# Kernel optimization log

Hardware: AMD Instinct MI355X
Metric: run time of the kernel (lower is better)

The kernel has to match this reference:

```python
import jax, jax.numpy as jnp
import numpy as np

EPS = 1e-12


def _complex_log(x):
    # log of a real tensor as a complex number: log|x| + i*pi*[x<0]
    real = jnp.log(jnp.maximum(jnp.abs(x), EPS))
    imag = jnp.where(x < 0, jnp.pi, 0.0).astype(jnp.float32)
    return jax.lax.complex(real.astype(jnp.float32), imag)


def _logcumsumexp_complex(x, axis):
    # numerically-stable complex logcumsumexp via associative scan
    def logaddexp_c(a, b):
        m = jnp.maximum(a.real, b.real)  # real-valued max for stability
        return jnp.log(jnp.exp(a - m) + jnp.exp(b - m)) + m
    return jax.lax.associative_scan(logaddexp_c, x, axis=axis)


def setup_inputs() -> dict:
    key = jax.random.key(0)
    ks = jax.random.split(key, 7)
    b, d, l, n = 2, 1024, 1024, 16
    u = jax.random.normal(ks[0], (b, d, l), dtype=jnp.float32)
    delta = jax.random.normal(ks[1], (b, d, l), dtype=jnp.float32)
    # A negative (like Mamba's A = -exp(A_log)) so the scan stays stable
    A = -(0.5 + jax.random.uniform(ks[2], (d, n), dtype=jnp.float32))
    B = jax.random.normal(ks[3], (b, n, l), dtype=jnp.float32)
    C = jax.random.normal(ks[4], (b, n, l), dtype=jnp.float32)
    D = jax.random.normal(ks[5], (d,), dtype=jnp.float32)
    z = jax.random.normal(ks[6], (b, d, l), dtype=jnp.float32)
    return {"u": u, "delta": delta, "A": A, "B": B, "C": C, "D": D, "z": z}


def reference(u, delta, A, B, C, D, z):
    # delta_softplus=True path of SelectiveScanTorch.forward
    dt = jax.nn.softplus(delta)                                   # (b,d,l)
    dA = jnp.einsum('bdl,dn->bldn', dt, A)                        # (b,l,d,n)
    dB_u = jnp.einsum('bdl,bdl,bnl->bldn', dt, u, B)              # (b,l,d,n)

    dB_u_log = _complex_log(dB_u)                                 # complex64
    # dA_star[l] = sum_{k=1}^{l} dA[k]  (exclusive of step 0, front-padded)
    dA_star = jnp.pad(jnp.cumsum(dA[:, 1:], axis=1),
                      ((0, 0), (1, 0), (0, 0), (0, 0)))
    x_log = _logcumsumexp_complex(dB_u_log - dA_star, axis=1) + dA_star

    x_real = jnp.exp(x_log.real) * jnp.cos(x_log.imag)            # (b,l,d,n)
    y = jnp.einsum('bldn,bnl->bdl', x_real.astype(C.dtype), C)    # (b,d,l)
    out = y + u * D[None, :, None]
    return (out * jax.nn.silu(z)).astype(u.dtype)
```

## Files before the change

### kernel.cpp

```cpp
#include <hip/hip_runtime.h>
#include <math.h>

namespace {

constexpr int kD = 1024;
constexpr int kL = 1024;
constexpr int kN = 16;
constexpr int kE = 8;
constexpr int kJ = 8;
constexpr int kT = 256;

__global__ __launch_bounds__(kT)
void selscan(const float* __restrict__ u,
             const float* __restrict__ delta,
             const float* __restrict__ A,
             const float* __restrict__ Bm,
             const float* __restrict__ Cm,
             const float* __restrict__ Dv,
             const float* __restrict__ z,
             float* __restrict__ out)
{
    __shared__ float2 sax[128][kN + 1];

    const int bd   = blockIdx.x;
    const int b    = bd >> 10;
    const int d    = bd & (kD - 1);
    const int t    = threadIdx.x;
    const int lane = t & 63;
    const int wave = t >> 6;
    const int nh   = t & 1;
    const int n0   = nh << 3;
    const int chunk = t >> 1;
    const int l0   = chunk << 3;
    const size_t base = (size_t)bd * kL;

    const float LOG2E = 1.4426950408889634f;
    const float LN2   = 0.6931471805599453f;

    float dt[kE], dtu[kE];
    {
        float4 d0 = *(const float4*)(delta + base + l0);
        float4 d1 = *(const float4*)(delta + base + l0 + 4);
        float4 u0 = *(const float4*)(u + base + l0);
        float4 u1 = *(const float4*)(u + base + l0 + 4);
        float dd[kE] = {d0.x,d0.y,d0.z,d0.w,d1.x,d1.y,d1.z,d1.w};
        float uu[kE] = {u0.x,u0.y,u0.z,u0.w,u1.x,u1.y,u1.z,u1.w};
        #pragma unroll
        for (int s = 0; s < kE; ++s) {
            float x = dd[s];
            float e = __builtin_amdgcn_exp2f(-fabsf(x) * LOG2E);
            float sp = fmaxf(x, 0.f) + __builtin_amdgcn_logf(1.f + e) * LN2;
            dt[s]  = sp;
            dtu[s] = sp * uu[s];
        }
    }

    float cj[kJ];
    {
        float4 a0 = *(const float4*)(A + d * kN + n0);
        float4 a1 = *(const float4*)(A + d * kN + n0 + 4);
        cj[0]=a0.x*LOG2E; cj[1]=a0.y*LOG2E; cj[2]=a0.z*LOG2E; cj[3]=a0.w*LOG2E;
        cj[4]=a1.x*LOG2E; cj[5]=a1.y*LOG2E; cj[6]=a1.z*LOG2E; cj[7]=a1.w*LOG2E;
    }

    float Q[kJ][kE];
    float y[kE] = {0.f,0.f,0.f,0.f,0.f,0.f,0.f,0.f};
    const int rowbase = (b << 4) + n0;
    #pragma unroll
    for (int j = 0; j < kJ; ++j) {
        const float* Bp = Bm + (size_t)(rowbase + j) * kL + l0;
        const float* Cp = Cm + (size_t)(rowbase + j) * kL + l0;
        float4 b0 = *(const float4*)Bp;
        float4 b1 = *(const float4*)(Bp + 4);
        float4 c0 = *(const float4*)Cp;
        float4 c1 = *(const float4*)(Cp + 4);
        float Bv[kE] = {b0.x,b0.y,b0.z,b0.w,b1.x,b1.y,b1.z,b1.w};
        float Cv[kE] = {c0.x,c0.y,c0.z,c0.w,c1.x,c1.y,c1.z,c1.w};
        float x = 0.f, p = 1.f;
        #pragma unroll
        for (int s = 0; s < kE; ++s) {
            float e = __builtin_amdgcn_exp2f(dt[s] * cj[j]);
            x = fmaf(e, x, dtu[s] * Bv[s]);
            p *= e;
            Q[j][s] = p * Cv[s];
            y[s] = fmaf(x, Cv[s], y[s]);
        }
        sax[chunk][n0 + j] = make_float2(p, x);
    }
    __syncthreads();

    if (wave == 0) {
        const int sn = lane & 15;
        const int q  = lane >> 4;
        const int cb = q << 5;
        float p = 1.f, c = 0.f;
        #pragma unroll 8
        for (int i = 0; i < 32; ++i) {
            float2 ax = sax[cb + i][sn];
            c = fmaf(ax.x, c, ax.y);
            p *= ax.x;
        }
        float Ag = p, Xg = c;
        {
            float ain = __shfl_up(Ag, 16, 64);
            float xin = __shfl_up(Xg, 16, 64);
            bool act = (lane >= 16);
            Xg = fmaf(Ag, act ? xin : 0.f, Xg);
            Ag *= act ? ain : 1.f;
            ain = __shfl_up(Ag, 32, 64);
            xin = __shfl_up(Xg, 32, 64);
            act = (lane >= 32);
            Xg = fmaf(Ag, act ? xin : 0.f, Xg);
            Ag *= act ? ain : 1.f;
        }
        float gx = __shfl_up(Xg, 16, 64);
        float cc = (lane >= 16) ? gx : 0.f;
        #pragma unroll 8
        for (int i = 0; i < 32; ++i) {
            float2 ax = sax[cb + i][sn];
            sax[cb + i][sn].x = cc;
            cc = fmaf(ax.x, cc, ax.y);
        }
    }
    __syncthreads();

    #pragma unroll
    for (int j = 0; j < kJ; ++j) {
        float carry = sax[chunk][n0 + j].x;
        #pragma unroll
        for (int s = 0; s < kE; ++s)
            y[s] = fmaf(carry, Q[j][s], y[s]);
    }

    #pragma unroll
    for (int s = 0; s < kE; ++s) y[s] += __shfl_xor(y[s], 1, 64);

    const float D_d = Dv[d];
    float y0, y1, y2, y3;
    if (nh == 0) { y0 = y[0]; y1 = y[1]; y2 = y[2]; y3 = y[3]; }
    else         { y0 = y[4]; y1 = y[5]; y2 = y[6]; y3 = y[7]; }

    const int eoff = l0 + nh * 4;
    float4 zv = *(const float4*)(z + base + eoff);
    float4 uv = *(const float4*)(u + base + eoff);
    float s0 = __builtin_amdgcn_rcpf(1.f + __builtin_amdgcn_exp2f(-zv.x * LOG2E));
    float s1 = __builtin_amdgcn_rcpf(1.f + __builtin_amdgcn_exp2f(-zv.y * LOG2E));
    float s2 = __builtin_amdgcn_rcpf(1.f + __builtin_amdgcn_exp2f(-zv.z * LOG2E));
    float s3 = __builtin_amdgcn_rcpf(1.f + __builtin_amdgcn_exp2f(-zv.w * LOG2E));
    float4 o;
    o.x = (y0 + uv.x * D_d) * zv.x * s0;
    o.y = (y1 + uv.y * D_d) * zv.y * s1;
    o.z = (y2 + uv.z * D_d) * zv.z * s2;
    o.w = (y3 + uv.w * D_d) * zv.w * s3;
    *(float4*)(out + base + eoff) = o;
}

}

extern "C" void kernel_launch(void* const* d_in, const int* in_sizes, int n_in,
                              void* d_out, int out_size, void* d_ws, size_t ws_size,
                              hipStream_t stream) {
    const float* u     = (const float*)d_in[0];
    const float* delta = (const float*)d_in[1];
    const float* A     = (const float*)d_in[2];
    const float* Bm    = (const float*)d_in[3];
    const float* Cm    = (const float*)d_in[4];
    const float* Dv    = (const float*)d_in[5];
    const float* z     = (const float*)d_in[6];
    float* out = (float*)d_out;

    dim3 grid(2 * kD);
    dim3 block(kT);
    hipLaunchKernelGGL(selscan, grid, block, 0, stream,
                       u, delta, A, Bm, Cm, Dv, z, out);
}
```

Before: 26.04 us.

## Split state dimension across four threads per chunk with 512-thread blocks

Each length chunk is now handled by four threads covering 4 state channels each, instead of two threads covering 8, and the block grows to 512 threads. This halves per-thread B/C loads and the size of the Q register array, lowering register pressure and raising the number of threads available to hide latency. The cost is computing softplus and delta*u redundantly four times instead of twice, plus an extra shuffle-reduce step. The epilogue now writes two outputs per thread and reuses u from registers instead of reloading it from global memory.

Result: slower. 47.81 us (+83.6%).

```diff
diff --git a/kernel.cpp b/kernel.cpp
--- a/kernel.cpp
+++ b/kernel.cpp
@@ -7,8 +7,8 @@
 constexpr int kL = 1024;
 constexpr int kN = 16;
 constexpr int kE = 8;
-constexpr int kJ = 8;
-constexpr int kT = 256;
+constexpr int kJ = 4;
+constexpr int kT = 512;
 
 __global__ __launch_bounds__(kT)
 void selscan(const float* __restrict__ u,
@@ -28,9 +28,9 @@
     const int t    = threadIdx.x;
     const int lane = t & 63;
     const int wave = t >> 6;
-    const int nh   = t & 1;
-    const int n0   = nh << 3;
-    const int chunk = t >> 1;
+    const int ng   = t & 3;
+    const int n0   = ng << 2;
+    const int chunk = t >> 2;
     const int l0   = chunk << 3;
     const size_t base = (size_t)bd * kL;
 
@@ -38,11 +38,12 @@
     const float LN2   = 0.6931471805599453f;
 
     float dt[kE], dtu[kE];
+    float4 u0, u1;
     {
         float4 d0 = *(const float4*)(delta + base + l0);
         float4 d1 = *(const float4*)(delta + base + l0 + 4);
-        float4 u0 = *(const float4*)(u + base + l0);
-        float4 u1 = *(const float4*)(u + base + l0 + 4);
+        u0 = *(const float4*)(u + base + l0);
+        u1 = *(const float4*)(u + base + l0 + 4);
         float dd[kE] = {d0.x,d0.y,d0.z,d0.w,d1.x,d1.y,d1.z,d1.w};
         float uu[kE] = {u0.x,u0.y,u0.z,u0.w,u1.x,u1.y,u1.z,u1.w};
         #pragma unroll
@@ -57,10 +58,8 @@
 
     float cj[kJ];
     {
-        float4 a0 = *(const float4*)(A + d * kN + n0);
-        float4 a1 = *(const float4*)(A + d * kN + n0 + 4);
-        cj[0]=a0.x*LOG2E; cj[1]=a0.y*LOG2E; cj[2]=a0.z*LOG2E; cj[3]=a0.w*LOG2E;
-        cj[4]=a1.x*LOG2E; cj[5]=a1.y*LOG2E; cj[6]=a1.z*LOG2E; cj[7]=a1.w*LOG2E;
+        float4 a4 = *(const float4*)(A + d * kN + n0);
+        cj[0]=a4.x*LOG2E; cj[1]=a4.y*LOG2E; cj[2]=a4.z*LOG2E; cj[3]=a4.w*LOG2E;
     }
 
     float Q[kJ][kE];
@@ -133,26 +132,26 @@
     }
 
     #pragma unroll
-    for (int s = 0; s < kE; ++s) y[s] += __shfl_xor(y[s], 1, 64);
+    for (int s = 0; s < kE; ++s) {
+        y[s] += __shfl_xor(y[s], 1, 64);
+        y[s] += __shfl_xor(y[s], 2, 64);
+    }
 
     const float D_d = Dv[d];
-    float y0, y1, y2, y3;
-    if (nh == 0) { y0 = y[0]; y1 = y[1]; y2 = y[2]; y3 = y[3]; }
-    else         { y0 = y[4]; y1 = y[5]; y2 = y[6]; y3 = y[7]; }
+    bool g2 = (ng & 2) != 0, g1 = (ng & 1) != 0;
+    float ya  = g2 ? (g1 ? y[6] : y[4]) : (g1 ? y[2] : y[0]);
+    float yb  = g2 ? (g1 ? y[7] : y[5]) : (g1 ? y[3] : y[1]);
+    float ue0 = g2 ? (g1 ? u1.z : u1.x) : (g1 ? u0.z : u0.x);
+    float ue1 = g2 ? (g1 ? u1.w : u1.y) : (g1 ? u0.w : u0.y);
 
-    const int eoff = l0 + nh * 4;
-    float4 zv = *(const float4*)(z + base + eoff);
-    float4 uv = *(const float4*)(u + base + eoff);
+    const int eo = 2 * t;
+    float2 zv = *(const float2*)(z + base + eo);
     float s0 = __builtin_amdgcn_rcpf(1.f + __builtin_amdgcn_exp2f(-zv.x * LOG2E));
     float s1 = __builtin_amdgcn_rcpf(1.f + __builtin_amdgcn_exp2f(-zv.y * LOG2E));
-    float s2 = __builtin_amdgcn_rcpf(1.f + __builtin_amdgcn_exp2f(-zv.z * LOG2E));
-    float s3 = __builtin_amdgcn_rcpf(1.f + __builtin_amdgcn_exp2f(-zv.w * LOG2E));
-    float4 o;
-    o.x = (y0 + uv.x * D_d) * zv.x * s0;
-    o.y = (y1 + uv.y * D_d) * zv.y * s1;
-    o.z = (y2 + uv.z * D_d) * zv.z * s2;
-    o.w = (y3 + uv.w * D_d) * zv.w * s3;
-    *(float4*)(out + base + eoff) = o;
+    float2 o;
+    o.x = (ya + ue0 * D_d) * zv.x * s0;
+    o.y = (yb + ue1 * D_d) * zv.y * s1;
+    *(float2*)(out + base + eo) = o;
 }
 
 }
```

## Recompute decay products from prefix dt sums instead of holding Q in registers

Applied to the files above, without the earlier changes.

Drops the 64-entry Q[j][s] register array that held cumulative decay times C across the block barrier. Instead it computes prefix sums of dt and, after the carry scan, recomputes each decay factor as exp2(T[s]*A) and reloads C from global memory. The u*D term is also computed early from the already-loaded u, so the second load of u is gone. The aim is lower register pressure and higher occupancy, at the cost of extra exp2 calls, a second read of C, and a small numerical difference from using exp of a sum instead of a product of exps.

New measurement: 31.12 us. 1.2x slower.

```diff
diff --git a/kernel.cpp b/kernel.cpp
--- a/kernel.cpp
+++ b/kernel.cpp
@@ -33,11 +33,15 @@
     const int chunk = t >> 1;
     const int l0   = chunk << 3;
     const size_t base = (size_t)bd * kL;
+    const int eoff = l0 + nh * 4;
 
     const float LOG2E = 1.4426950408889634f;
     const float LN2   = 0.6931471805599453f;
 
+    const float D_d = Dv[d];
+
     float dt[kE], dtu[kE];
+    float ue0, ue1, ue2, ue3;
     {
         float4 d0 = *(const float4*)(delta + base + l0);
         float4 d1 = *(const float4*)(delta + base + l0 + 4);
@@ -53,7 +57,16 @@
             dt[s]  = sp;
             dtu[s] = sp * uu[s];
         }
+        ue0 = (nh ? u1.x : u0.x) * D_d;
+        ue1 = (nh ? u1.y : u0.y) * D_d;
+        ue2 = (nh ? u1.z : u0.z) * D_d;
+        ue3 = (nh ? u1.w : u0.w) * D_d;
     }
+
+    float T[kE];
+    T[0] = dt[0];
+    #pragma unroll
+    for (int s = 1; s < kE; ++s) T[s] = T[s - 1] + dt[s];
 
     float cj[kJ];
     {
@@ -63,7 +76,6 @@
         cj[4]=a1.x*LOG2E; cj[5]=a1.y*LOG2E; cj[6]=a1.z*LOG2E; cj[7]=a1.w*LOG2E;
     }
 
-    float Q[kJ][kE];
     float y[kE] = {0.f,0.f,0.f,0.f,0.f,0.f,0.f,0.f};
     const int rowbase = (b << 4) + n0;
     #pragma unroll
@@ -76,16 +88,15 @@
         float4 c1 = *(const float4*)(Cp + 4);
         float Bv[kE] = {b0.x,b0.y,b0.z,b0.w,b1.x,b1.y,b1.z,b1.w};
         float Cv[kE] = {c0.x,c0.y,c0.z,c0.w,c1.x,c1.y,c1.z,c1.w};
-        float x = 0.f, p = 1.f;
+        float x = 0.f;
         #pragma unroll
         for (int s = 0; s < kE; ++s) {
             float e = __builtin_amdgcn_exp2f(dt[s] * cj[j]);
             x = fmaf(e, x, dtu[s] * Bv[s]);
-            p *= e;
-            Q[j][s] = p * Cv[s];
             y[s] = fmaf(x, Cv[s], y[s]);
         }
-        sax[chunk][n0 + j] = make_float2(p, x);
+        float a = __builtin_amdgcn_exp2f(T[kE - 1] * cj[j]);
+        sax[chunk][n0 + j] = make_float2(a, x);
     }
     __syncthreads();
 
@@ -126,32 +137,36 @@
 
     #pragma unroll
     for (int j = 0; j < kJ; ++j) {
+        const float* Cp = Cm + (size_t)(rowbase + j) * kL + l0;
+        float4 c0 = *(const float4*)Cp;
+        float4 c1 = *(const float4*)(Cp + 4);
+        float Cv[kE] = {c0.x,c0.y,c0.z,c0.w,c1.x,c1.y,c1.z,c1.w};
         float carry = sax[chunk][n0 + j].x;
         #pragma unroll
-        for (int s = 0; s < kE; ++s)
-            y[s] = fmaf(carry, Q[j][s], y[s]);
+        for (int s = 0; s < kE; ++s) {
+            float p = __builtin_amdgcn_exp2f(T[s] * cj[j]);
+            y[s] = fmaf(carry * p, Cv[s], y[s]);
+        }
     }
 
     #pragma unroll
     for (int s = 0; s < kE; ++s) y[s] += __shfl_xor(y[s], 1, 64);
 
-    const float D_d = Dv[d];
-    float y0, y1, y2, y3;
-    if (nh == 0) { y0 = y[0]; y1 = y[1]; y2 = y[2]; y3 = y[3]; }
-    else         { y0 = y[4]; y1 = y[5]; y2 = y[6]; y3 = y[7]; }
+    float y0 = nh ? y[4] : y[0];
+    float y1 = nh ? y[5] : y[1];
+    float y2 = nh ? y[6] : y[2];
+    float y3 = nh ? y[7] : y[3];
 
-    const int eoff = l0 + nh * 4;
     float4 zv = *(const float4*)(z + base + eoff);
-    float4 uv = *(const float4*)(u + base + eoff);
     float s0 = __builtin_amdgcn_rcpf(1.f + __builtin_amdgcn_exp2f(-zv.x * LOG2E));
     float s1 = __builtin_amdgcn_rcpf(1.f + __builtin_amdgcn_exp2f(-zv.y * LOG2E));
     float s2 = __builtin_amdgcn_rcpf(1.f + __builtin_amdgcn_exp2f(-zv.z * LOG2E));
     float s3 = __builtin_amdgcn_rcpf(1.f + __builtin_amdgcn_exp2f(-zv.w * LOG2E));
     float4 o;
-    o.x = (y0 + uv.x * D_d) * zv.x * s0;
-    o.y = (y1 + uv.y * D_d) * zv.y * s1;
-    o.z = (y2 + uv.z * D_d) * zv.z * s2;
-    o.w = (y3 + uv.w * D_d) * zv.w * s3;
+    o.x = (y0 + ue0) * zv.x * s0;
+    o.y = (y1 + ue1) * zv.y * s1;
+    o.z = (y2 + ue2) * zv.z * s2;
+    o.w = (y3 + ue3) * zv.w * s3;
     *(float4*)(out + base + eoff) = o;
 }
 
```

## Parallelize chunk-carry scan across all four waves with cross-wave combine

Applied to the files above, without the earlier changes.

The inter-chunk carry scan previously ran on wave 0 alone, with each lane walking 32 chunks serially in two passes. Now all four waves each take 32 chunks, split 8 per lane group, then combine their partial results through a small shared array and an extra barrier. This shortens the serial carry-propagation phase while the other waves would otherwise sit idle, at the cost of one more __syncthreads and a little extra shared memory traffic.

Result: slower. 27.51 us (+5.7%).

```diff
diff --git a/kernel.cpp b/kernel.cpp
--- a/kernel.cpp
+++ b/kernel.cpp
@@ -21,6 +21,7 @@
              float* __restrict__ out)
 {
     __shared__ float2 sax[128][kN + 1];
+    __shared__ float2 sw[4][kN];
 
     const int bd   = blockIdx.x;
     const int b    = bd >> 10;
@@ -89,34 +90,45 @@
     }
     __syncthreads();
 
-    if (wave == 0) {
+    {
         const int sn = lane & 15;
         const int q  = lane >> 4;
-        const int cb = q << 5;
+        const int cb = (wave << 5) + (q << 3);
+
         float p = 1.f, c = 0.f;
-        #pragma unroll 8
-        for (int i = 0; i < 32; ++i) {
+        #pragma unroll
+        for (int i = 0; i < 8; ++i) {
             float2 ax = sax[cb + i][sn];
             c = fmaf(ax.x, c, ax.y);
             p *= ax.x;
         }
-        float Ag = p, Xg = c;
+        float Aq = p, Xq = c;
         {
-            float ain = __shfl_up(Ag, 16, 64);
-            float xin = __shfl_up(Xg, 16, 64);
+            float ain = __shfl_up(Aq, 16, 64);
+            float xin = __shfl_up(Xq, 16, 64);
             bool act = (lane >= 16);
-            Xg = fmaf(Ag, act ? xin : 0.f, Xg);
-            Ag *= act ? ain : 1.f;
-            ain = __shfl_up(Ag, 32, 64);
-            xin = __shfl_up(Xg, 32, 64);
+            Xq = fmaf(Aq, act ? xin : 0.f, Xq);
+            Aq *= act ? ain : 1.f;
+            ain = __shfl_up(Aq, 32, 64);
+            xin = __shfl_up(Xq, 32, 64);
             act = (lane >= 32);
-            Xg = fmaf(Ag, act ? xin : 0.f, Xg);
-            Ag *= act ? ain : 1.f;
+            Xq = fmaf(Aq, act ? xin : 0.f, Xq);
+            Aq *= act ? ain : 1.f;
         }
-        float gx = __shfl_up(Xg, 16, 64);
-        float cc = (lane >= 16) ? gx : 0.f;
-        #pragma unroll 8
-        for (int i = 0; i < 32; ++i) {
+        if (q == 3) sw[wave][sn] = make_float2(Aq, Xq);
+        float eA = __shfl_up(Aq, 16, 64);
+        float eX = __shfl_up(Xq, 16, 64);
+        if (lane < 16) { eA = 1.f; eX = 0.f; }
+        __syncthreads();
+        float wx = 0.f;
+        if (wave > 0) {
+            wx = sw[0][sn].y;
+            if (wave > 1) { float2 s1 = sw[1][sn]; wx = fmaf(s1.x, wx, s1.y); }
+            if (wave > 2) { float2 s2 = sw[2][sn]; wx = fmaf(s2.x, wx, s2.y); }
+        }
+        float cc = fmaf(eA, wx, eX);
+        #pragma unroll
+        for (int i = 0; i < 8; ++i) {
             float2 ax = sax[cb + i][sn];
             sax[cb + i][sn].x = cc;
             cc = fmaf(ax.x, cc, ax.y);
```
